# Kernel tuning notes

Hardware: AMD Instinct MI355X
Metric: run time of the kernel (lower is better)

The kernel has to match this reference:

```python
import jax, jax.numpy as jnp
import numpy as np

DIM = 1024
HEADS = 16
EPS = 1e-05
B, T, C, H, W = 2, 16, DIM, 32, 32


def setup_inputs() -> dict:
    key = jax.random.key(0)
    ks = jax.random.split(key, 4)
    s = 1.0 / np.sqrt(DIM)
    return {
        "x": jax.random.normal(ks[0], (B, T, C, H, W), dtype=jnp.float32),
        "ln_w": jnp.ones((C,), dtype=jnp.float32),
        "ln_b": jnp.zeros((C,), dtype=jnp.float32),
        "Wq": jax.random.normal(ks[1], (C, C), dtype=jnp.float32) * s,
        "Wk": jax.random.normal(ks[2], (C, C), dtype=jnp.float32) * s,
        "Wv": jax.random.normal(ks[3], (C, C), dtype=jnp.float32) * s,
    }


def reference(x, ln_w, ln_b, Wq, Wk, Wv):
    b, t, c, h, w = x.shape
    heads = HEADS
    dh = c // heads
    scale = dh ** (-0.5)

    # Channel LayerNorm: normalize over C per (b,t,h,w)
    xc = jnp.transpose(x, (0, 1, 3, 4, 2))  # [B,T,H,W,C]
    mu = jnp.mean(xc, axis=-1, keepdims=True)
    var = jnp.mean(jnp.square(xc - mu), axis=-1, keepdims=True)
    xn = (xc - mu) * jax.lax.rsqrt(var + EPS) * ln_w + ln_b  # [B,T,H,W,C]

    # Q/K from spatial mean-pool
    pooled = jnp.mean(xn, axis=(2, 3))  # [B,T,C]
    q = pooled @ Wq.T  # [B,T,C]
    k = pooled @ Wk.T  # [B,T,C]

    # V per pixel; torch permutes to [B,W,H,T,C] then flattens W-major
    v = jnp.transpose(xn, (0, 3, 2, 1, 4)).reshape(b, h * w, t, c)  # [B,HW(w-major),T,C]
    v = v @ Wv.T

    q = q.reshape(b, t, heads, dh).transpose(0, 2, 1, 3) * scale  # [B,h,T,dh]
    k = k.reshape(b, t, heads, dh).transpose(0, 2, 3, 1)          # [B,h,dh,T]
    v = v.reshape(b, h * w, t, heads, dh).transpose(0, 1, 3, 2, 4)  # [B,HW,h,T,dh]

    attn = jax.nn.softmax(jnp.matmul(q, k), axis=-1)  # [B,h,T,T]
    out = jnp.einsum('bhst,bnhtd->bnhsd', attn, v)    # [B,HW,h,T,dh]
    # permute(0,3,2,4,1) -> [B,T,h,dh,HW], then view as (H,W)
    out = out.transpose(0, 3, 2, 4, 1).reshape(b, t, c, h, w)
    return out
```

## Files before the change

### kernel.cpp

```cpp
#include <hip/hip_runtime.h>
#include <stdint.h>
#include <stddef.h>

#define CDIM 1024
#define HWD  1024
#define TD   16
#define BD   2
#define NH   16
#define DHD  64

typedef __attribute__((ext_vector_type(8))) short bf16x8;
typedef __attribute__((ext_vector_type(4))) short bf16x4;
typedef __attribute__((ext_vector_type(4))) float f32x4;

static __device__ __forceinline__ short f2bf(float f) {
  uint32_t u = __builtin_bit_cast(uint32_t, f);
  uint32_t r = (u + 0x7FFFu + ((u >> 16) & 1u)) >> 16;
  return (short)(uint16_t)r;
}
static __device__ __forceinline__ float bf2f(short s) {
  return __builtin_bit_cast(float, (uint32_t)((uint16_t)s) << 16);
}

static __device__ __forceinline__ void gl_lds16(const short* g, short* l) {
  __builtin_amdgcn_global_load_lds((const __attribute__((address_space(1))) unsigned int*)g,
                                   (__attribute__((address_space(3))) unsigned int*)l,
                                   16, 0, 0);
}

__global__ void k_cast3(const float* __restrict__ Wq, const float* __restrict__ Wk,
                        const float* __restrict__ Wv, short* __restrict__ Wqkb,
                        short* __restrict__ Wb) {
  int bid = blockIdx.x;
  int mat = bid >> 10;
  const float* src = mat == 0 ? Wq : (mat == 1 ? Wk : Wv);
  short* dst = mat == 0 ? Wqkb : (mat == 1 ? Wqkb + 1048576 : Wb);
  int i = ((bid & 1023) * 256 + threadIdx.x) * 4;
  f32x4 v = *(const f32x4*)&src[i];
  dst[i + 0] = f2bf(v[0]);
  dst[i + 1] = f2bf(v[1]);
  dst[i + 2] = f2bf(v[2]);
  dst[i + 3] = f2bf(v[3]);
}

__global__ __launch_bounds__(512) void k_ln(const float* __restrict__ x,
                                            const float* __restrict__ lnw,
                                            const float* __restrict__ lnb,
                                            short* __restrict__ xnT,
                                            float* __restrict__ part) {
  int bt = blockIdx.y;
  int pg = blockIdx.x;
  int P0 = pg * 64;
  int tid = threadIdx.x;
  int pq = tid & 15, cr = tid >> 4;
  int pbase = P0 + pq * 4;
  const float* xs = x + (size_t)bt * CDIM * HWD;
  short* outB = xnT + (size_t)bt * CDIM * HWD;

  __shared__ __align__(16) char lbuf[2 * 32 * 65 * 4];
  float* redA = (float*)lbuf;
  float* redB = redA + 32 * 65;
  short* tile = (short*)lbuf;
  __shared__ float muS[64], rsS[64];

  float s[4] = {}, s2[4] = {};
  #pragma unroll
  for (int j = 0; j < 32; ++j) {
    int c = cr + 32 * j;
    f32x4 v = *(const f32x4*)&xs[(size_t)c * HWD + pbase];
    #pragma unroll
    for (int i = 0; i < 4; ++i) { s[i] += v[i]; s2[i] += v[i] * v[i]; }
  }
  #pragma unroll
  for (int i = 0; i < 4; ++i) {
    redA[cr * 65 + pq * 4 + i] = s[i];
    redB[cr * 65 + pq * 4 + i] = s2[i];
  }
  __syncthreads();
  if (tid < 64) {
    float a = 0.f, b2 = 0.f;
    #pragma unroll
    for (int k = 0; k < 32; ++k) { a += redA[k * 65 + tid]; b2 += redB[k * 65 + tid]; }
    float mu = a * (1.0f / CDIM);
    float var = b2 * (1.0f / CDIM) - mu * mu;
    muS[tid] = mu;
    rsS[tid] = rsqrtf(var + 1e-5f);
  }
  __syncthreads();
  float mu_[4], rs_[4];
  #pragma unroll
  for (int i = 0; i < 4; ++i) { mu_[i] = muS[pq * 4 + i]; rs_[i] = rsS[pq * 4 + i]; }

  for (int h = 0; h < 8; ++h) {
    #pragma unroll
    for (int jj = 0; jj < 4; ++jj) {
      int cl = cr + 32 * jj;
      int c = h * 128 + cl;
      f32x4 v = *(const f32x4*)&xs[(size_t)c * HWD + pbase];
      float w = lnw[c], bb = lnb[c];
      int cc = cl >> 3, c7 = cl & 7;
      float psum = 0.f;
      #pragma unroll
      for (int i = 0; i < 4; ++i) {
        int px = pq * 4 + i;
        float xn = (v[i] - mu_[i]) * rs_[i] * w + bb;
        psum += xn;
        tile[px * 130 + ((cc ^ (px & 7)) << 3) + c7] = f2bf(xn);
      }
      psum += __shfl_xor(psum, 1, 64);
      psum += __shfl_xor(psum, 2, 64);
      psum += __shfl_xor(psum, 4, 64);
      psum += __shfl_xor(psum, 8, 64);
      if (pq == 0)
        part[((size_t)(bt * 16 + pg)) * CDIM + c] = psum;
    }
    __syncthreads();
    {
      int qr = tid & 63, sg = tid >> 6;
      int q = (qr & 31) * 32 + pg * 2 + (qr >> 5);
      short* dst = outB + (size_t)q * CDIM + h * 128 + sg * 16;
      #pragma unroll
      for (int mm = 0; mm < 2; ++mm) {
        int cc = sg * 2 + mm;
        bf16x8 vv = *(const bf16x8*)&tile[qr * 130 + ((cc ^ (qr & 7)) << 3)];
        *(bf16x8*)&dst[mm * 8] = vv;
      }
    }
    __syncthreads();
  }
}

__global__ void k_pool_red(const float* __restrict__ part, short* __restrict__ pooledb) {
  int bt = blockIdx.y;
  int c = blockIdx.x * 256 + threadIdx.x;
  float s = 0.f;
  #pragma unroll
  for (int pc = 0; pc < 16; ++pc) s += part[((size_t)(bt * 16 + pc)) * CDIM + c];
  pooledb[bt * CDIM + c] = f2bf(s * (1.0f / HWD));
}

__global__ __launch_bounds__(256) void k_qk_mfma(const short* __restrict__ Wqkb,
                                                 const short* __restrict__ pooledb,
                                                 float* __restrict__ qm,
                                                 float* __restrict__ km) {
  int n0 = blockIdx.x * 128;
  __shared__ __align__(16) short lA[32 * 32];
  __shared__ __align__(16) short lB[128 * 32];
  int tid = threadIdx.x, lane = tid & 63, wid = tid >> 6;
  int s0 = wid * 128 + lane, s1 = s0 + 64;
  int fr = lane & 15, fk = (lane >> 4) * 8;
  f32x4 acc[2][2] = {};

  for (int kt = 0; kt < CDIM / 32; ++kt) {
    int k0 = kt * 32;
    __syncthreads();
    gl_lds16(&Wqkb[(size_t)(n0 + (s0 >> 2)) * CDIM + k0 + (s0 & 3) * 8], &lB[s0 * 8]);
    gl_lds16(&Wqkb[(size_t)(n0 + (s1 >> 2)) * CDIM + k0 + (s1 & 3) * 8], &lB[s1 * 8]);
    if (wid < 2) {
      gl_lds16(&pooledb[(size_t)(tid >> 2) * CDIM + k0 + (tid & 3) * 8], &lA[tid * 8]);
    }
    __syncthreads();
    bf16x8 af[2], bfr[2];
    #pragma unroll
    for (int mi = 0; mi < 2; ++mi)
      af[mi] = *(const bf16x8*)&lA[(mi * 16 + fr) * 32 + fk];
    #pragma unroll
    for (int ni = 0; ni < 2; ++ni)
      bfr[ni] = *(const bf16x8*)&lB[(wid * 32 + ni * 16 + fr) * 32 + fk];
    #pragma unroll
    for (int mi = 0; mi < 2; ++mi)
      #pragma unroll
      for (int ni = 0; ni < 2; ++ni)
        acc[mi][ni] = __builtin_amdgcn_mfma_f32_16x16x32_bf16(af[mi], bfr[ni], acc[mi][ni], 0, 0, 0);
  }

  int cr = lane >> 4;
  #pragma unroll
  for (int mi = 0; mi < 2; ++mi)
    #pragma unroll
    for (int ni = 0; ni < 2; ++ni)
      #pragma unroll
      for (int rr = 0; rr < 4; ++rr) {
        int row = mi * 16 + cr * 4 + rr;
        int col = n0 + wid * 32 + ni * 16 + fr;
        float v = acc[mi][ni][rr];
        if (col < 1024) qm[(size_t)row * CDIM + col] = v;
        else            km[(size_t)row * CDIM + col - 1024] = v;
      }
}

__global__ void k_attn(const float* __restrict__ qm, const float* __restrict__ km,
                       float* __restrict__ attn) {
  int bg = blockIdx.x;
  int b = bg >> 4, g = bg & 15;
  int s = threadIdx.x >> 4, t = threadIdx.x & 15;
  const float* qr = qm + (size_t)(b * TD + s) * CDIM + g * DHD;
  const float* kr = km + (size_t)(b * TD + t) * CDIM + g * DHD;
  float d = 0.f;
  #pragma unroll
  for (int i = 0; i < DHD; ++i) d += qr[i] * kr[i];
  d *= 0.125f;
  float m = d;
  #pragma unroll
  for (int off = 8; off; off >>= 1) m = fmaxf(m, __shfl_xor(m, off, 16));
  float e = __expf(d - m);
  float sum = e;
  #pragma unroll
  for (int off = 8; off; off >>= 1) sum += __shfl_xor(sum, off, 16);
  attn[(size_t)bg * 256 + s * 16 + t] = e / sum;
}

__global__ __launch_bounds__(256) void k_vgemm(const short* __restrict__ Wb,
                                               const short* __restrict__ xnT,
                                               short* __restrict__ vp) {
  int bt = blockIdx.z;
  int m0 = blockIdx.y * 128;
  int n0 = blockIdx.x * 128;
  const short* A = Wb;
  const short* Bm = xnT + (size_t)bt * CDIM * HWD;
  __shared__ __align__(16) short lA[128 * 32];
  __shared__ __align__(16) short lB[128 * 32];
  int tid = threadIdx.x;
  int lane = tid & 63;
  int wid = tid >> 6;
  int wr = (wid >> 1) * 64;
  int wc = (wid & 1) * 64;
  f32x4 acc[4][4] = {};

  int sm = tid >> 2;
  int slc = ((tid & 3) ^ ((tid >> 3) & 3)) * 8;
  const short* gA = A + (size_t)(m0 + sm) * CDIM + slc;
  const short* gB = Bm + (size_t)(n0 + sm) * CDIM + slc;
  short* dA = &lA[tid * 8];
  short* dB = &lB[tid * 8];
  int fr = lane & 15;
  int c0 = (((lane >> 4) ^ ((fr >> 1) & 3)) * 8);

  for (int kt = 0; kt < CDIM / 32; ++kt) {
    __syncthreads();
    gl_lds16(gA + kt * 32, dA);
    gl_lds16(gA + kt * 32 + (size_t)64 * CDIM, dA + 64 * 32);
    gl_lds16(gB + kt * 32, dB);
    gl_lds16(gB + kt * 32 + (size_t)64 * CDIM, dB + 64 * 32);
    __syncthreads();
    bf16x8 af[4], bfr[4];
    #pragma unroll
    for (int mi = 0; mi < 4; ++mi)
      af[mi] = *(const bf16x8*)&lA[(wr + mi * 16 + fr) * 32 + c0];
    #pragma unroll
    for (int ni = 0; ni < 4; ++ni)
      bfr[ni] = *(const bf16x8*)&lB[(wc + ni * 16 + fr) * 32 + c0];
    #pragma unroll
    for (int mi = 0; mi < 4; ++mi)
      #pragma unroll
      for (int ni = 0; ni < 4; ++ni)
        acc[mi][ni] = __builtin_amdgcn_mfma_f32_16x16x32_bf16(af[mi], bfr[ni], acc[mi][ni], 0, 0, 0);
  }

  short* outB = vp + (size_t)bt * CDIM * HWD;
  int cr = lane >> 4;
  #pragma unroll
  for (int mi = 0; mi < 4; ++mi)
    #pragma unroll
    for (int ni = 0; ni < 4; ++ni)
      #pragma unroll
      for (int r = 0; r < 4; ++r) {
        int row = m0 + wr + mi * 16 + cr * 4 + r;
        int col = n0 + wc + ni * 16 + fr;
        outB[(size_t)row * HWD + col] = f2bf(acc[mi][ni][r]);
      }
}

__global__ __launch_bounds__(256) void k_mix(const short* __restrict__ vp,
                                             const float* __restrict__ attn,
                                             float* __restrict__ out) {
  int c = blockIdx.x;
  int b = blockIdx.y;
  int g = c >> 6;
  __shared__ __align__(16) short vpl[TD * HWD];
  __shared__ float at[256];
  int tid = threadIdx.x;
  at[tid] = attn[(size_t)(b * NH + g) * 256 + tid];
  #pragma unroll
  for (int j = 0; j < 8; ++j) {
    int chunk = j * 256 + tid;
    int t = chunk >> 7, qc = chunk & 127;
    bf16x8 v = *(const bf16x8*)&vp[((size_t)(b * TD + t) * CDIM + c) * HWD + qc * 8];
    *(bf16x8*)&vpl[t * HWD + qc * 8] = v;
  }
  __syncthreads();
  int p = tid * 4;
  #pragma unroll
  for (int sh = 0; sh < 2; ++sh) {
    f32x4 acc[8] = {};
    #pragma unroll
    for (int t = 0; t < TD; ++t) {
      bf16x4 v4 = *(const bf16x4*)&vpl[t * HWD + p];
      f32x4 vf = {bf2f(v4[0]), bf2f(v4[1]), bf2f(v4[2]), bf2f(v4[3])};
      #pragma unroll
      for (int s8 = 0; s8 < 8; ++s8) {
        float a = at[(sh * 8 + s8) * 16 + t];
        acc[s8] += a * vf;
      }
    }
    #pragma unroll
    for (int s8 = 0; s8 < 8; ++s8) {
      int s = sh * 8 + s8;
      *(f32x4*)&out[((size_t)(b * TD + s) * CDIM + c) * HWD + p] = acc[s8];
    }
  }
}

extern "C" void kernel_launch(void* const* d_in, const int* in_sizes, int n_in,
                              void* d_out, int out_size, void* d_ws, size_t ws_size,
                              hipStream_t stream) {
  const float* x   = (const float*)d_in[0];
  const float* lnw = (const float*)d_in[1];
  const float* lnb = (const float*)d_in[2];
  const float* Wq  = (const float*)d_in[3];
  const float* Wk  = (const float*)d_in[4];
  const float* Wv  = (const float*)d_in[5];
  float* out = (float*)d_out;

  char* ws = (char*)d_ws;
  const size_t XNT_OFF   = 0;
  const size_t VP_OFF    = XNT_OFF + 67108864;
  const size_t WB_OFF    = VP_OFF + 67108864;
  const size_t WQKB_OFF  = WB_OFF + 2097152;
  const size_t POOLB_OFF = WQKB_OFF + 4194304;
  const size_t QM_OFF    = POOLB_OFF + 65536;
  const size_t KM_OFF    = QM_OFF + 131072;
  const size_t ATTN_OFF  = KM_OFF + 131072;

  short* xnT    = (short*)(ws + XNT_OFF);
  short* vp     = (short*)(ws + VP_OFF);
  float* part   = (float*)(ws + VP_OFF);
  short* Wb     = (short*)(ws + WB_OFF);
  short* Wqkb   = (short*)(ws + WQKB_OFF);
  short* poolb  = (short*)(ws + POOLB_OFF);
  float* qm     = (float*)(ws + QM_OFF);
  float* km     = (float*)(ws + KM_OFF);
  float* attn   = (float*)(ws + ATTN_OFF);

  k_cast3<<<dim3(3072), 256, 0, stream>>>(Wq, Wk, Wv, Wqkb, Wb);
  k_ln<<<dim3(16, 32), 512, 0, stream>>>(x, lnw, lnb, xnT, part);
  k_pool_red<<<dim3(4, 32), 256, 0, stream>>>(part, poolb);
  k_qk_mfma<<<dim3(16), 256, 0, stream>>>(Wqkb, poolb, qm, km);
  k_attn<<<dim3(32), 256, 0, stream>>>(qm, km, attn);
  k_vgemm<<<dim3(8, 8, 32), 256, 0, stream>>>(Wb, xnT, vp);
  k_mix<<<dim3(1024, 2), 256, 0, stream>>>(vp, attn, out);
}
```

Measured before the change: 211.4 us.

## Restructure LayerNorm kernel to one pixel per lane, dropping LDS transpose

The LayerNorm kernel now gives each lane one pixel and each wave a 256-channel slice, cutting the block to 256 threads. Each thread writes 8 contiguous bf16 channels of the transposed output directly, and the pooled partial sums come from full-wave shuffle reductions. This removes the LDS transpose tile and its barriers. In exchange, global loads are scalar 4-byte loads instead of float4, the transposed stores scatter 16-byte chunks across rows, and there are many more shuffles per element.

```diff
diff --git a/kernel.cpp b/kernel.cpp
--- a/kernel.cpp
+++ b/kernel.cpp
@@ -43,90 +43,68 @@
   dst[i + 3] = f2bf(v[3]);
 }
 
-__global__ __launch_bounds__(512) void k_ln(const float* __restrict__ x,
+__global__ __launch_bounds__(256) void k_ln(const float* __restrict__ x,
                                             const float* __restrict__ lnw,
                                             const float* __restrict__ lnb,
                                             short* __restrict__ xnT,
                                             float* __restrict__ part) {
   int bt = blockIdx.y;
-  int pg = blockIdx.x;
-  int P0 = pg * 64;
+  int pgrp = blockIdx.x;
   int tid = threadIdx.x;
-  int pq = tid & 15, cr = tid >> 4;
-  int pbase = P0 + pq * 4;
+  int lane = tid & 63, w = tid >> 6;
+  int p = pgrp * 64 + lane;
   const float* xs = x + (size_t)bt * CDIM * HWD;
   short* outB = xnT + (size_t)bt * CDIM * HWD;
 
-  __shared__ __align__(16) char lbuf[2 * 32 * 65 * 4];
-  float* redA = (float*)lbuf;
-  float* redB = redA + 32 * 65;
-  short* tile = (short*)lbuf;
+  float s = 0.f, s2 = 0.f;
+  #pragma unroll 8
+  for (int j = 0; j < 256; ++j) {
+    float v = xs[(size_t)(w * 256 + j) * HWD + p];
+    s += v; s2 += v * v;
+  }
+  __shared__ float redA[4][72], redB[4][72];
   __shared__ float muS[64], rsS[64];
-
-  float s[4] = {}, s2[4] = {};
-  #pragma unroll
-  for (int j = 0; j < 32; ++j) {
-    int c = cr + 32 * j;
-    f32x4 v = *(const f32x4*)&xs[(size_t)c * HWD + pbase];
-    #pragma unroll
-    for (int i = 0; i < 4; ++i) { s[i] += v[i]; s2[i] += v[i] * v[i]; }
-  }
-  #pragma unroll
-  for (int i = 0; i < 4; ++i) {
-    redA[cr * 65 + pq * 4 + i] = s[i];
-    redB[cr * 65 + pq * 4 + i] = s2[i];
-  }
+  redA[w][lane] = s;
+  redB[w][lane] = s2;
   __syncthreads();
   if (tid < 64) {
-    float a = 0.f, b2 = 0.f;
-    #pragma unroll
-    for (int k = 0; k < 32; ++k) { a += redA[k * 65 + tid]; b2 += redB[k * 65 + tid]; }
+    float a  = redA[0][tid] + redA[1][tid] + redA[2][tid] + redA[3][tid];
+    float b2 = redB[0][tid] + redB[1][tid] + redB[2][tid] + redB[3][tid];
     float mu = a * (1.0f / CDIM);
     float var = b2 * (1.0f / CDIM) - mu * mu;
     muS[tid] = mu;
     rsS[tid] = rsqrtf(var + 1e-5f);
   }
   __syncthreads();
-  float mu_[4], rs_[4];
-  #pragma unroll
-  for (int i = 0; i < 4; ++i) { mu_[i] = muS[pq * 4 + i]; rs_[i] = rsS[pq * 4 + i]; }
-
-  for (int h = 0; h < 8; ++h) {
-    #pragma unroll
-    for (int jj = 0; jj < 4; ++jj) {
-      int cl = cr + 32 * jj;
-      int c = h * 128 + cl;
-      f32x4 v = *(const f32x4*)&xs[(size_t)c * HWD + pbase];
-      float w = lnw[c], bb = lnb[c];
-      int cc = cl >> 3, c7 = cl & 7;
-      float psum = 0.f;
-      #pragma unroll
-      for (int i = 0; i < 4; ++i) {
-        int px = pq * 4 + i;
-        float xn = (v[i] - mu_[i]) * rs_[i] * w + bb;
-        psum += xn;
-        tile[px * 130 + ((cc ^ (px & 7)) << 3) + c7] = f2bf(xn);
-      }
-      psum += __shfl_xor(psum, 1, 64);
-      psum += __shfl_xor(psum, 2, 64);
-      psum += __shfl_xor(psum, 4, 64);
-      psum += __shfl_xor(psum, 8, 64);
-      if (pq == 0)
-        part[((size_t)(bt * 16 + pg)) * CDIM + c] = psum;
-    }
-    __syncthreads();
-    {
-      int qr = tid & 63, sg = tid >> 6;
-      int q = (qr & 31) * 32 + pg * 2 + (qr >> 5);
-      short* dst = outB + (size_t)q * CDIM + h * 128 + sg * 16;
-      #pragma unroll
-      for (int mm = 0; mm < 2; ++mm) {
-        int cc = sg * 2 + mm;
-        bf16x8 vv = *(const bf16x8*)&tile[qr * 130 + ((cc ^ (qr & 7)) << 3)];
-        *(bf16x8*)&dst[mm * 8] = vv;
-      }
-    }
-    __syncthreads();
+  float mu = muS[lane], rs = rsS[lane];
+
+  int q = (p & 31) * 32 + (p >> 5);
+  short* dstRow = outB + (size_t)q * CDIM;
+  float* partRow = part + ((size_t)(bt * 16 + pgrp)) * CDIM;
+
+  for (int ch = 0; ch < 32; ++ch) {
+    int c0 = w * 256 + ch * 8;
+    float xn[8];
+    #pragma unroll
+    for (int j = 0; j < 8; ++j) {
+      float v = xs[(size_t)(c0 + j) * HWD + p];
+      xn[j] = (v - mu) * rs * lnw[c0 + j] + lnb[c0 + j];
+    }
+    bf16x8 pack;
+    #pragma unroll
+    for (int j = 0; j < 8; ++j) pack[j] = f2bf(xn[j]);
+    *(bf16x8*)&dstRow[c0] = pack;
+    #pragma unroll
+    for (int j = 0; j < 8; ++j) {
+      float ps = xn[j];
+      ps += __shfl_xor(ps, 1, 64);
+      ps += __shfl_xor(ps, 2, 64);
+      ps += __shfl_xor(ps, 4, 64);
+      ps += __shfl_xor(ps, 8, 64);
+      ps += __shfl_xor(ps, 16, 64);
+      ps += __shfl_xor(ps, 32, 64);
+      if (lane == j) partRow[c0 + j] = ps;
+    }
   }
 }
 
@@ -343,7 +321,7 @@
   float* attn   = (float*)(ws + ATTN_OFF);
 
   k_cast3<<<dim3(3072), 256, 0, stream>>>(Wq, Wk, Wv, Wqkb, Wb);
-  k_ln<<<dim3(16, 32), 512, 0, stream>>>(x, lnw, lnb, xnT, part);
+  k_ln<<<dim3(16, 32), 256, 0, stream>>>(x, lnw, lnb, xnT, part);
   k_pool_red<<<dim3(4, 32), 256, 0, stream>>>(part, poolb);
   k_qk_mfma<<<dim3(16), 256, 0, stream>>>(Wqkb, poolb, qm, km);
   k_attn<<<dim3(32), 256, 0, stream>>>(qm, km, attn);
```

Measured after the change: 259.0 us. +22.5%, slower.
